# Kernel optimization log

Measured on AMD Instinct MI355X. Metric: run time of the kernel, lower is better.

## Reference

```python
import jax, jax.numpy as jnp
import numpy as np

B, C, H, W = 8, 256, 128, 128
NW = 512  # n_weights (depthwise multiplier 2)
EPS = 1e-5
SPARSITY = 0.5


def setup_inputs() -> dict:
    key = jax.random.key(0)
    k_x, k_sign, k_mask, k_w1 = jax.random.split(key, 4)
    x = jax.random.normal(k_x, (B, C, H, W), dtype=jnp.float32)
    gamma = jnp.ones((C,), dtype=jnp.float32)
    beta = jnp.zeros((C,), dtype=jnp.float32)
    # frozen binary/sparse LBP depthwise weights in {-1, 0, +1}
    sign = jax.random.bernoulli(k_sign, 0.5, (NW, 1, 3, 3)).astype(jnp.float32) * 2.0 - 1.0
    inactive = jax.random.uniform(k_mask, (NW, 1, 3, 3)) > SPARSITY
    lbp_w = jnp.where(inactive, 0.0, sign)
    # 1x1 conv params (PyTorch default init scale)
    bound = 1.0 / np.sqrt(NW)
    w1 = jax.random.uniform(k_w1, (C, NW, 1, 1), minval=-bound, maxval=bound, dtype=jnp.float32)
    b1 = jnp.zeros((C,), dtype=jnp.float32)
    return {"x": x, "gamma": gamma, "beta": beta, "lbp_w": lbp_w, "w1": w1, "b1": b1}


def reference(x, gamma, beta, lbp_w, w1, b1):
    # BatchNorm2d in training mode: biased batch stats over (N, H, W)
    mean = jnp.mean(x, axis=(0, 2, 3), keepdims=True)
    var = jnp.var(x, axis=(0, 2, 3), keepdims=True)
    xn = (x - mean) * jax.lax.rsqrt(var + EPS)
    xn = xn * gamma[None, :, None, None] + beta[None, :, None, None]
    # depthwise 3x3 conv, padding=1, groups=C (depth multiplier NW//C)
    y = jax.lax.conv_general_dilated(
        xn, lbp_w, window_strides=(1, 1), padding=((1, 1), (1, 1)),
        dimension_numbers=("NCHW", "OIHW", "NCHW"), feature_group_count=C)
    y = jax.nn.relu(y)
    # 1x1 conv NW -> C plus bias, then residual add
    z = jax.lax.conv_general_dilated(
        y, w1, window_strides=(1, 1), padding=((0, 0), (0, 0)),
        dimension_numbers=("NCHW", "OIHW", "NCHW"))
    z = z + b1[None, :, None, None]
    return z + x
```

## Files before the change

### kernel.cpp

```cpp
#include <hip/hip_runtime.h>

#define B_ 8
#define C_ 256
#define H_ 128
#define W_ 128
#define NW_ 512
#define HW_ (H_*W_)
#define EPS_ 1e-5f

typedef __attribute__((ext_vector_type(8))) short bf16x8;
typedef __attribute__((ext_vector_type(4))) float f32x4;

__device__ __forceinline__ unsigned short f2bf(float f) {
  unsigned u = __float_as_uint(f);
  u += 0x7fffu + ((u >> 16) & 1u);
  return (unsigned short)(u >> 16);
}
__device__ __forceinline__ float bf2f(unsigned short h) {
  return __uint_as_float(((unsigned)h) << 16);
}
__device__ __forceinline__ float bflo(unsigned u) { return __uint_as_float(u << 16); }
__device__ __forceinline__ float bfhi(unsigned u) { return __uint_as_float(u & 0xffff0000u); }

__global__ __launch_bounds__(256)
void bn_partial(const float* __restrict__ x, float* __restrict__ psum,
                float* __restrict__ psq) {
  const int b = blockIdx.x, c = blockIdx.y, tid = threadIdx.x;
  const float4* p = (const float4*)(x + (size_t)(b*C_ + c) * HW_);
  float s = 0.f, s2 = 0.f;
  #pragma unroll
  for (int i = 0; i < 16; ++i) {
    float4 v = p[tid + i*256];
    s  += v.x + v.y + v.z + v.w;
    s2 += v.x*v.x + v.y*v.y + v.z*v.z + v.w*v.w;
  }
  #pragma unroll
  for (int off = 32; off > 0; off >>= 1) {
    s  += __shfl_down(s, off);
    s2 += __shfl_down(s2, off);
  }
  __shared__ float rs[4], rq[4];
  if ((tid & 63) == 0) { rs[tid >> 6] = s; rq[tid >> 6] = s2; }
  __syncthreads();
  if (tid == 0) {
    float S = rs[0]+rs[1]+rs[2]+rs[3], S2 = rq[0]+rq[1]+rq[2]+rq[3];
    psum[c*B_ + b] = S;
    psq [c*B_ + b] = S2;
  }
}

__global__ __launch_bounds__(256)
void bn_final(float* __restrict__ wsf, const float* __restrict__ gamma,
              const float* __restrict__ beta) {
  const int c = threadIdx.x;
  float S = 0.f, S2 = 0.f;
  #pragma unroll
  for (int b = 0; b < B_; ++b) { S += wsf[512 + c*B_ + b]; S2 += wsf[2560 + c*B_ + b]; }
  const float n = (float)(B_*HW_);
  float mean = S / n;
  float var  = S2 / n - mean*mean;
  float scl  = gamma[c] * rsqrtf(var + EPS_);
  wsf[c]       = scl;
  wsf[C_ + c]  = beta[c] - mean*scl;
}

__global__ __launch_bounds__(64)
void w1prep(const float* __restrict__ w1, ushort* __restrict__ w1f) {
  const int l15 = threadIdx.x & 15, quad = threadIdx.x >> 4;
  const int mtG = blockIdx.x >> 4, ks = blockIdx.x & 15;
  const float* src = w1 + (size_t)(mtG*16 + l15)*NW_ + ks*32 + quad*8;
  float4 f0 = *(const float4*)src, f1 = *(const float4*)(src + 4);
  union { unsigned u[4]; uint4 q; } cv;
  cv.u[0] = (unsigned)f2bf(f0.x) | ((unsigned)f2bf(f0.y) << 16);
  cv.u[1] = (unsigned)f2bf(f0.z) | ((unsigned)f2bf(f0.w) << 16);
  cv.u[2] = (unsigned)f2bf(f1.x) | ((unsigned)f2bf(f1.y) << 16);
  cv.u[3] = (unsigned)f2bf(f1.z) | ((unsigned)f2bf(f1.w) << 16);
  ((uint4*)w1f)[blockIdx.x*64 + threadIdx.x] = cv.q;
}

template<bool PREW1>
__global__ __launch_bounds__(256, 3)
void fused_mfma(const float* __restrict__ x, const float* __restrict__ lbpw,
                const float* __restrict__ w1raw, const ushort* __restrict__ w1f,
                const float* __restrict__ b1, const float* __restrict__ sc_sh,
                float* __restrict__ out) {
  const int tid  = threadIdx.x;
  const int b    = blockIdx.z;
  const int h0   = blockIdx.y * 4;
  const int w0   = blockIdx.x * 16;
  const int wave = tid >> 6;
  const int lane = tid & 63;
  const int l15  = lane & 15;
  const int quad = lane >> 4;
  const int cl   = tid >> 4;
  const int jj   = tid & 15;

  __shared__ float  s_scale[C_];
  __shared__ float  s_shift[C_];
  __shared__ float  s_b1[C_];
  __shared__ __align__(16) float  s_xn[2][16][6][20];
  __shared__ __align__(16) ushort s_yT[2][64][40];
  __shared__ __align__(8)  ushort s_wall[NW_][12];

  s_scale[tid] = sc_sh[tid];
  s_shift[tid] = sc_sh[C_ + tid];
  s_b1[tid]    = b1[tid];

  int geo[7];
  unsigned actmask = 0, padmask = 0;
  #pragma unroll
  for (int k = 0; k < 7; ++k) {
    geo[k] = 0;
    const int e = jj + 16*k;
    if (e < 108) {
      const int r   = e / 18;
      const int col = e - r*18;
      const int lofs = cl*120 + r*20 + col;
      const int h = h0 + r - 1;
      const int w = w0 + col - 1;
      if (h >= 0 && h < H_ && w >= 0 && w < W_) {
        actmask |= (1u << k);
        geo[k] = ((cl*HW_ + h*W_ + w) << 11) | lofs;
      } else {
        padmask |= (1u << k);
        geo[k] = lofs;
      }
    }
  }
  {
    float* p0 = &s_xn[0][0][0][0];
    float* p1 = &s_xn[1][0][0][0];
    #pragma unroll
    for (int k = 0; k < 7; ++k)
      if (padmask & (1u << k)) { p0[geo[k] & 2047] = 0.f; p1[geo[k] & 2047] = 0.f; }
  }

  f32x4 acc[4][4];
  #pragma unroll
  for (int mt = 0; mt < 4; ++mt)
    #pragma unroll
    for (int nt = 0; nt < 4; ++nt) { f32x4 z = {0.f,0.f,0.f,0.f}; acc[mt][nt] = z; }

  __syncthreads();

  #pragma unroll
  for (int rr = 0; rr < 2; ++rr) {
    const int row = tid + rr*256;
    const float* wp = lbpw + (size_t)row*9;
    #pragma unroll
    for (int j = 0; j < 9; ++j) s_wall[row][j] = f2bf(wp[j]);
  }
  {
    const float scl = s_scale[cl];
    const float sh  = s_shift[cl];
    const float* xc = x + (size_t)(b*C_) * HW_;
    float* xb = &s_xn[0][0][0][0];
    #pragma unroll
    for (int k = 0; k < 7; ++k)
      if (actmask & (1u << k)) xb[geo[k] & 2047] = fmaf(xc[geo[k] >> 11], scl, sh);
  }
  __syncthreads();

  #pragma unroll 2
  for (int kc = 0; kc < 16; ++kc) {
    const int p = kc & 1;

    uint4 w1q[4];
    if constexpr (PREW1) {
      #pragma unroll
      for (int mt = 0; mt < 4; ++mt)
        w1q[mt] = *(const uint4*)(w1f + (size_t)(((wave*4 + mt)*16 + kc)*64 + lane)*8);
    }

    float reg[7];
    if (kc < 15) {
      const float* xc = x + (size_t)(b*C_ + (kc + 1)*16) * HW_;
      #pragma unroll
      for (int k = 0; k < 7; ++k)
        if (actmask & (1u << k)) reg[k] = xc[geo[k] >> 11];
    }

    {
      const ushort* wr0 = &s_wall[kc*32 + 2*cl][0];
      const ushort* wr1 = &s_wall[kc*32 + 2*cl + 1][0];
      const uint2 qa0 = *(const uint2*)(wr0);
      const uint2 qa1 = *(const uint2*)(wr0 + 4);
      const unsigned qa2 = *(const unsigned*)(wr0 + 8);
      const uint2 qb0 = *(const uint2*)(wr1);
      const uint2 qb1 = *(const uint2*)(wr1 + 4);
      const unsigned qb2 = *(const unsigned*)(wr1 + 8);
      const float wA[9] = { bflo(qa0.x), bfhi(qa0.x), bflo(qa0.y), bfhi(qa0.y),
                            bflo(qa1.x), bfhi(qa1.x), bflo(qa1.y), bfhi(qa1.y),
                            bflo(qa2) };
      const float wB[9] = { bflo(qb0.x), bfhi(qb0.x), bflo(qb0.y), bfhi(qb0.y),
                            bflo(qb1.x), bfhi(qb1.x), bflo(qb1.y), bfhi(qb1.y),
                            bflo(qb2) };
      float a0[4] = {0.f,0.f,0.f,0.f}, a1[4] = {0.f,0.f,0.f,0.f};
      #pragma unroll
      for (int rr = 0; rr < 6; ++rr) {
        const float v0 = s_xn[p][cl][rr][jj];
        const float v1 = s_xn[p][cl][rr][jj + 1];
        const float v2 = s_xn[p][cl][rr][jj + 2];
        #pragma unroll
        for (int r = 0; r < 4; ++r) {
          const int di = rr - r;
          if (di >= 0 && di < 3) {
            a0[r] = fmaf(wA[di*3+2], v2, fmaf(wA[di*3+1], v1, fmaf(wA[di*3+0], v0, a0[r])));
            a1[r] = fmaf(wB[di*3+2], v2, fmaf(wB[di*3+1], v1, fmaf(wB[di*3+0], v0, a1[r])));
          }
        }
      }
      #pragma unroll
      for (int r = 0; r < 4; ++r) {
        const unsigned pk = (unsigned)f2bf(fmaxf(a0[r], 0.f)) |
                            ((unsigned)f2bf(fmaxf(a1[r], 0.f)) << 16);
        *(unsigned*)&s_yT[p][r*16 + jj][2*cl] = pk;
      }
    }

    if (kc < 15) {
      const int c1 = (kc + 1) * 16 + cl;
      const float scl = s_scale[c1];
      const float sh  = s_shift[c1];
      float* xb = &s_xn[p ^ 1][0][0][0];
      #pragma unroll
      for (int k = 0; k < 7; ++k)
        if (actmask & (1u << k)) xb[geo[k] & 2047] = fmaf(reg[k], scl, sh);
    }

    __syncthreads();

    bf16x8 bfr[4];
    #pragma unroll
    for (int nt = 0; nt < 4; ++nt)
      bfr[nt] = *(const bf16x8*)&s_yT[p][nt*16 + l15][quad*8];

    #pragma unroll
    for (int mt = 0; mt < 4; ++mt) {
      bf16x8 afr;
      if constexpr (PREW1) {
        union { uint4 q; bf16x8 v; } cv;
        cv.q = w1q[mt];
        afr = cv.v;
      } else {
        const float* wp = w1raw + (size_t)(wave*64 + mt*16 + l15)*NW_ + kc*32 + quad*8;
        const float4 f0 = *(const float4*)wp;
        const float4 f1 = *(const float4*)(wp + 4);
        union { unsigned u[4]; bf16x8 v; } cv;
        cv.u[0] = (unsigned)f2bf(f0.x) | ((unsigned)f2bf(f0.y) << 16);
        cv.u[1] = (unsigned)f2bf(f0.z) | ((unsigned)f2bf(f0.w) << 16);
        cv.u[2] = (unsigned)f2bf(f1.x) | ((unsigned)f2bf(f1.y) << 16);
        cv.u[3] = (unsigned)f2bf(f1.z) | ((unsigned)f2bf(f1.w) << 16);
        afr = cv.v;
      }
      #pragma unroll
      for (int nt = 0; nt < 4; ++nt)
        acc[mt][nt] = __builtin_amdgcn_mfma_f32_16x16x32_bf16(afr, bfr[nt], acc[mt][nt], 0, 0, 0);
    }
  }

  #pragma unroll
  for (int mt = 0; mt < 4; ++mt) {
    #pragma unroll
    for (int nt = 0; nt < 4; ++nt) {
      const int h = h0 + nt;
      #pragma unroll
      for (int i = 0; i < 4; ++i) {
        const int ch = wave*64 + mt*16 + quad*4 + i;
        const size_t o = ((size_t)(b*C_ + ch)*H_ + h)*W_ + (w0 + l15);
        out[o] = acc[mt][nt][i] + s_b1[ch] + x[o];
      }
    }
  }
}

extern "C" void kernel_launch(void* const* d_in, const int* in_sizes, int n_in,
                              void* d_out, int out_size, void* d_ws, size_t ws_size,
                              hipStream_t stream) {
  const float* x     = (const float*)d_in[0];
  const float* gamma = (const float*)d_in[1];
  const float* beta  = (const float*)d_in[2];
  const float* lbpw  = (const float*)d_in[3];
  const float* w1    = (const float*)d_in[4];
  const float* b1    = (const float*)d_in[5];
  float* out = (float*)d_out;

  float* wsf = (float*)d_ws;
  ushort* w1f = (ushort*)((char*)d_ws + 18432);
  const bool pre = ws_size >= (size_t)(18432 + 262144);

  bn_partial<<<dim3(B_, C_), 256, 0, stream>>>(x, wsf + 512, wsf + 2560);
  bn_final<<<1, 256, 0, stream>>>(wsf, gamma, beta);

  dim3 grid(W_/16, H_/4, B_);
  if (pre) {
    w1prep<<<256, 64, 0, stream>>>(w1, w1f);
    fused_mfma<true><<<grid, 256, 0, stream>>>(x, lbpw, w1, w1f, b1, wsf, out);
  } else {
    fused_mfma<false><<<grid, 256, 0, stream>>>(x, lbpw, w1, w1f, b1, wsf, out);
  }
}
```

Before: 362.7 us.

## Stream raw x tiles via global_load_lds and fold BN affine after depthwise conv

Raw input tiles now go straight from global memory into LDS through async global_load_lds, waited on with explicit vmcnt. This replaces the register round-trip and the per-element BN fmaf on the way in. The BN scale and shift are applied after the depthwise conv, using the precomputed tap-sum shift term, and border columns are zeroed in registers. It also swizzles the yT LDS layout to avoid bank conflicts, seeds the accumulators with the bias, and raises occupancy to 4 blocks per SM. The risks are hand-managed waitcnt counts, the edge handling near the start of the buffer, and changed numerics from applying the affine after the convolution.

```diff
diff --git a/kernel.cpp b/kernel.cpp
--- a/kernel.cpp
+++ b/kernel.cpp
@@ -7,6 +7,7 @@
 #define NW_ 512
 #define HW_ (H_*W_)
 #define EPS_ 1e-5f
+#define GLIM_ (B_*C_*HW_ - 4)
 
 typedef __attribute__((ext_vector_type(8))) short bf16x8;
 typedef __attribute__((ext_vector_type(4))) float f32x4;
@@ -16,11 +17,13 @@
   u += 0x7fffu + ((u >> 16) & 1u);
   return (unsigned short)(u >> 16);
 }
-__device__ __forceinline__ float bf2f(unsigned short h) {
-  return __uint_as_float(((unsigned)h) << 16);
-}
 __device__ __forceinline__ float bflo(unsigned u) { return __uint_as_float(u << 16); }
 __device__ __forceinline__ float bfhi(unsigned u) { return __uint_as_float(u & 0xffff0000u); }
+
+__device__ __forceinline__ void gld_lds16(const float* g, float* l) {
+  __builtin_amdgcn_global_load_lds((const __attribute__((address_space(1))) void*)g,
+                                   (__attribute__((address_space(3))) void*)l, 16, 0, 0);
+}
 
 __global__ __launch_bounds__(256)
 void bn_partial(const float* __restrict__ x, float* __restrict__ psum,
@@ -79,7 +82,7 @@
 }
 
 template<bool PREW1>
-__global__ __launch_bounds__(256, 3)
+__global__ __launch_bounds__(256, 4)
 void fused_mfma(const float* __restrict__ x, const float* __restrict__ lbpw,
                 const float* __restrict__ w1raw, const ushort* __restrict__ w1f,
                 const float* __restrict__ b1, const float* __restrict__ sc_sh,
@@ -88,78 +91,87 @@
   const int b    = blockIdx.z;
   const int h0   = blockIdx.y * 4;
   const int w0   = blockIdx.x * 16;
-  const int wave = tid >> 6;
+  const int wv   = tid >> 6;
   const int lane = tid & 63;
   const int l15  = lane & 15;
   const int quad = lane >> 4;
   const int cl   = tid >> 4;
   const int jj   = tid & 15;
 
-  __shared__ float  s_scale[C_];
-  __shared__ float  s_shift[C_];
-  __shared__ float  s_b1[C_];
-  __shared__ __align__(16) float  s_xn[2][16][6][20];
-  __shared__ __align__(16) ushort s_yT[2][64][40];
-  __shared__ __align__(8)  ushort s_wall[NW_][12];
-
-  s_scale[tid] = sc_sh[tid];
-  s_shift[tid] = sc_sh[C_ + tid];
-  s_b1[tid]    = b1[tid];
-
-  int geo[7];
-  unsigned actmask = 0, padmask = 0;
-  #pragma unroll
-  for (int k = 0; k < 7; ++k) {
-    geo[k] = 0;
-    const int e = jj + 16*k;
-    if (e < 108) {
-      const int r   = e / 18;
-      const int col = e - r*18;
-      const int lofs = cl*120 + r*20 + col;
-      const int h = h0 + r - 1;
-      const int w = w0 + col - 1;
-      if (h >= 0 && h < H_ && w >= 0 && w < W_) {
-        actmask |= (1u << k);
-        geo[k] = ((cl*HW_ + h*W_ + w) << 11) | lofs;
+  __shared__ __align__(16) float    s_xn[2][1920];
+  __shared__ __align__(16) ushort   s_yT[2][64][40];
+  __shared__ __align__(16) ushort   s_wpA[256][16];
+  __shared__ __align__(16) unsigned s_wpB[256];
+  __shared__ __align__(16) float    s_cc[768];
+
+  {
+    const float* wp0 = lbpw + (size_t)(2*tid)*9;
+    float S0 = 0.f, S1 = 0.f;
+    #pragma unroll
+    for (int t = 0; t < 9; ++t) {
+      const float we = wp0[t], wo = wp0[9 + t];
+      S0 += we; S1 += wo;
+      if (t < 8) {
+        s_wpA[tid][2*t]   = f2bf(we);
+        s_wpA[tid][2*t+1] = f2bf(wo);
       } else {
-        padmask |= (1u << k);
-        geo[k] = lofs;
-      }
-    }
-  }
+        s_wpB[tid] = (unsigned)f2bf(we) | ((unsigned)f2bf(wo) << 16);
+      }
+    }
+    const float scl = sc_sh[tid];
+    const float sh  = sc_sh[C_ + tid];
+    s_cc[tid*3 + 0] = scl;
+    s_cc[tid*3 + 1] = sh * S0;
+    s_cc[tid*3 + 2] = sh * S1;
+  }
+
+  const int S0i = wv*120 + lane;
+  const int ch0 = S0i/30, re0 = S0i - ch0*30;
+  const int r0 = re0/5, q0 = re0 - r0*5;
+  const int hh0 = h0 - 1 + r0;
+  const bool v0 = (hh0 >= 0) && (hh0 < H_);
+  const int gSb0 = ((b*C_ + ch0)*HW_) + hh0*W_ + (w0 - 1) + 4*q0;
+  const bool hasS1 = (lane < 56);
+  const int S1i = wv*120 + 64 + lane;
+  const int ch1 = S1i/30, re1 = S1i - ch1*30;
+  const int r1 = re1/5, q1 = re1 - r1*5;
+  const int hh1 = h0 - 1 + r1;
+  const bool v1 = hasS1 && (hh1 >= 0) && (hh1 < H_);
+  const int gSb1 = ((b*C_ + ch1)*HW_) + hh1*W_ + (w0 - 1) + 4*q1;
+
   {
-    float* p0 = &s_xn[0][0][0][0];
-    float* p1 = &s_xn[1][0][0][0];
-    #pragma unroll
-    for (int k = 0; k < 7; ++k)
-      if (padmask & (1u << k)) { p0[geo[k] & 2047] = 0.f; p1[geo[k] & 2047] = 0.f; }
+    const float4 z4 = {0.f, 0.f, 0.f, 0.f};
+    if (!v0) { *(float4*)&s_xn[0][S0i*4] = z4; *(float4*)&s_xn[1][S0i*4] = z4; }
+    if (hasS1 && !v1) { *(float4*)&s_xn[0][S1i*4] = z4; *(float4*)&s_xn[1][S1i*4] = z4; }
   }
 
   f32x4 acc[4][4];
   #pragma unroll
-  for (int mt = 0; mt < 4; ++mt)
-    #pragma unroll
-    for (int nt = 0; nt < 4; ++nt) { f32x4 z = {0.f,0.f,0.f,0.f}; acc[mt][nt] = z; }
+  for (int mt = 0; mt < 4; ++mt) {
+    const f32x4 bv = *(const f32x4*)(b1 + wv*64 + mt*16 + quad*4);
+    #pragma unroll
+    for (int nt = 0; nt < 4; ++nt) acc[mt][nt] = bv;
+  }
 
   __syncthreads();
 
-  #pragma unroll
-  for (int rr = 0; rr < 2; ++rr) {
-    const int row = tid + rr*256;
-    const float* wp = lbpw + (size_t)row*9;
-    #pragma unroll
-    for (int j = 0; j < 9; ++j) s_wall[row][j] = f2bf(wp[j]);
-  }
+  const bool patch = v0 && (gSb0 < 0);
   {
-    const float scl = s_scale[cl];
-    const float sh  = s_shift[cl];
-    const float* xc = x + (size_t)(b*C_) * HW_;
-    float* xb = &s_xn[0][0][0][0];
-    #pragma unroll
-    for (int k = 0; k < 7; ++k)
-      if (actmask & (1u << k)) xb[geo[k] & 2047] = fmaf(xc[geo[k] >> 11], scl, sh);
-  }
-  __syncthreads();
+    float* lb = &s_xn[0][wv*480];
+    if (v0 && !patch) gld_lds16(x + gSb0, lb);
+    if (v1)           gld_lds16(x + gSb1, lb + 256);
+    if (patch) {
+      s_xn[0][S0i*4 + 0] = 0.f;
+      s_xn[0][S0i*4 + 1] = x[0];
+      s_xn[0][S0i*4 + 2] = x[1];
+      s_xn[0][S0i*4 + 3] = x[2];
+    }
+  }
+
+  const bool killL = (blockIdx.x == 0) && (jj == 0);
+  const bool killR = (blockIdx.x == (W_/16 - 1)) && (jj == 15);
+  const int  uofs  = ((cl >> 2) ^ (jj & 3))*8 + 2*(cl & 3);
+  const int  rofs  = (quad ^ (l15 & 3))*8;
 
   #pragma unroll 2
   for (int kc = 0; kc < 16; ++kc) {
@@ -169,71 +181,67 @@
     if constexpr (PREW1) {
       #pragma unroll
       for (int mt = 0; mt < 4; ++mt)
-        w1q[mt] = *(const uint4*)(w1f + (size_t)(((wave*4 + mt)*16 + kc)*64 + lane)*8);
-    }
-
-    float reg[7];
+        w1q[mt] = *(const uint4*)(w1f + (size_t)(((wv*4 + mt)*16 + kc)*64 + lane)*8);
+    }
+    __builtin_amdgcn_sched_barrier(0);
+
     if (kc < 15) {
-      const float* xc = x + (size_t)(b*C_ + (kc + 1)*16) * HW_;
-      #pragma unroll
-      for (int k = 0; k < 7; ++k)
-        if (actmask & (1u << k)) reg[k] = xc[geo[k] >> 11];
-    }
+      const int coff = (kc + 1)*(16*HW_);
+      float* lb = &s_xn[p ^ 1][wv*480];
+      int ga = gSb0 + coff; if (ga > GLIM_) ga = GLIM_;
+      if (v0) gld_lds16(x + ga, lb);
+      int gb = gSb1 + coff; if (gb > GLIM_) gb = GLIM_;
+      if (v1) gld_lds16(x + gb, lb + 256);
+    }
+    __builtin_amdgcn_sched_barrier(0);
+
+    if (kc < 15) asm volatile("s_waitcnt vmcnt(6)" ::: "memory");
+    else         asm volatile("s_waitcnt vmcnt(4)" ::: "memory");
+    __builtin_amdgcn_sched_barrier(0);
 
     {
-      const ushort* wr0 = &s_wall[kc*32 + 2*cl][0];
-      const ushort* wr1 = &s_wall[kc*32 + 2*cl + 1][0];
-      const uint2 qa0 = *(const uint2*)(wr0);
-      const uint2 qa1 = *(const uint2*)(wr0 + 4);
-      const unsigned qa2 = *(const unsigned*)(wr0 + 8);
-      const uint2 qb0 = *(const uint2*)(wr1);
-      const uint2 qb1 = *(const uint2*)(wr1 + 4);
-      const unsigned qb2 = *(const unsigned*)(wr1 + 8);
-      const float wA[9] = { bflo(qa0.x), bfhi(qa0.x), bflo(qa0.y), bfhi(qa0.y),
-                            bflo(qa1.x), bfhi(qa1.x), bflo(qa1.y), bfhi(qa1.y),
-                            bflo(qa2) };
-      const float wB[9] = { bflo(qb0.x), bfhi(qb0.x), bflo(qb0.y), bfhi(qb0.y),
-                            bflo(qb1.x), bfhi(qb1.x), bflo(qb1.y), bfhi(qb1.y),
-                            bflo(qb2) };
-      float a0[4] = {0.f,0.f,0.f,0.f}, a1[4] = {0.f,0.f,0.f,0.f};
+      const int cinG = kc*16 + cl;
+      const uint4 wa = *(const uint4*)&s_wpA[cinG][0];
+      const uint4 wb = *(const uint4*)&s_wpA[cinG][8];
+      const unsigned w8 = s_wpB[cinG];
+      const unsigned wt[9] = { wa.x, wa.y, wa.z, wa.w, wb.x, wb.y, wb.z, wb.w, w8 };
+      const float* cp = &s_cc[cinG*3];
+      const float scl = cp[0], sb0 = cp[1], sb1 = cp[2];
+
+      float A0[4] = {0.f,0.f,0.f,0.f}, A1[4] = {0.f,0.f,0.f,0.f};
+      const float* xb = &s_xn[p][cl*120 + jj];
       #pragma unroll
       for (int rr = 0; rr < 6; ++rr) {
-        const float v0 = s_xn[p][cl][rr][jj];
-        const float v1 = s_xn[p][cl][rr][jj + 1];
-        const float v2 = s_xn[p][cl][rr][jj + 2];
+        float va = xb[rr*20 + 0];
+        const float vb = xb[rr*20 + 1];
+        float vc = xb[rr*20 + 2];
+        if (killL) va = 0.f;
+        if (killR) vc = 0.f;
         #pragma unroll
         for (int r = 0; r < 4; ++r) {
           const int di = rr - r;
           if (di >= 0 && di < 3) {
-            a0[r] = fmaf(wA[di*3+2], v2, fmaf(wA[di*3+1], v1, fmaf(wA[di*3+0], v0, a0[r])));
-            a1[r] = fmaf(wB[di*3+2], v2, fmaf(wB[di*3+1], v1, fmaf(wB[di*3+0], v0, a1[r])));
+            A0[r] = fmaf(bflo(wt[di*3+2]), vc, fmaf(bflo(wt[di*3+1]), vb, fmaf(bflo(wt[di*3+0]), va, A0[r])));
+            A1[r] = fmaf(bfhi(wt[di*3+2]), vc, fmaf(bfhi(wt[di*3+1]), vb, fmaf(bfhi(wt[di*3+0]), va, A1[r])));
           }
         }
       }
       #pragma unroll
       for (int r = 0; r < 4; ++r) {
-        const unsigned pk = (unsigned)f2bf(fmaxf(a0[r], 0.f)) |
-                            ((unsigned)f2bf(fmaxf(a1[r], 0.f)) << 16);
-        *(unsigned*)&s_yT[p][r*16 + jj][2*cl] = pk;
-      }
-    }
-
-    if (kc < 15) {
-      const int c1 = (kc + 1) * 16 + cl;
-      const float scl = s_scale[c1];
-      const float sh  = s_shift[c1];
-      float* xb = &s_xn[p ^ 1][0][0][0];
-      #pragma unroll
-      for (int k = 0; k < 7; ++k)
-        if (actmask & (1u << k)) xb[geo[k] & 2047] = fmaf(reg[k], scl, sh);
-    }
-
-    __syncthreads();
+        const float y0 = fmaxf(fmaf(scl, A0[r], sb0), 0.f);
+        const float y1 = fmaxf(fmaf(scl, A1[r], sb1), 0.f);
+        *(unsigned*)&s_yT[p][r*16 + jj][uofs] =
+            (unsigned)f2bf(y0) | ((unsigned)f2bf(y1) << 16);
+      }
+    }
+
+    asm volatile("s_waitcnt lgkmcnt(0)" ::: "memory");
+    __builtin_amdgcn_s_barrier();
 
     bf16x8 bfr[4];
     #pragma unroll
     for (int nt = 0; nt < 4; ++nt)
-      bfr[nt] = *(const bf16x8*)&s_yT[p][nt*16 + l15][quad*8];
+      bfr[nt] = *(const bf16x8*)&s_yT[p][nt*16 + l15][rofs];
 
     #pragma unroll
     for (int mt = 0; mt < 4; ++mt) {
@@ -243,7 +251,7 @@
         cv.q = w1q[mt];
         afr = cv.v;
       } else {
-        const float* wp = w1raw + (size_t)(wave*64 + mt*16 + l15)*NW_ + kc*32 + quad*8;
+        const float* wp = w1raw + (size_t)(wv*64 + mt*16 + l15)*NW_ + kc*32 + quad*8;
         const float4 f0 = *(const float4*)wp;
         const float4 f1 = *(const float4*)(wp + 4);
         union { unsigned u[4]; bf16x8 v; } cv;
@@ -266,9 +274,9 @@
       const int h = h0 + nt;
       #pragma unroll
       for (int i = 0; i < 4; ++i) {
-        const int ch = wave*64 + mt*16 + quad*4 + i;
+        const int ch = wv*64 + mt*16 + quad*4 + i;
         const size_t o = ((size_t)(b*C_ + ch)*H_ + h)*W_ + (w0 + l15);
-        out[o] = acc[mt][nt][i] + s_b1[ch] + x[o];
+        out[o] = acc[mt][nt][i] + x[o];
       }
     }
   }
```

Result: slower. 394.4 us (+8.7%).
